# Performance work log

Measured on AMD Instinct MI355X. Metric: run time of the kernel, lower is better.

## Reference

```python
import jax, jax.numpy as jnp
import numpy as np

C = 66  # channels (joints)
NB_CLASSES = 14
T = 96


def conv1d(x, w, b, pad, groups=1):
    # x: (N, Cin, L), w: (Cout, Cin//groups, K)
    y = jax.lax.conv_general_dilated(
        x, w, window_strides=(1,), padding=[(pad, pad)],
        feature_group_count=groups, dimension_numbers=('NCH', 'OIH', 'NCH'))
    return y + b[None, :, None]


def pool2(x):
    # AvgPool1d(kernel_size=2) along last axis
    return x.reshape(*x.shape[:-1], x.shape[-1] // 2, 2).mean(-1)


def setup_inputs() -> dict:
    key = jax.random.key(0)
    ks = jax.random.split(key, 16)

    def xavier(k, shape, fan_in, fan_out, gain=jnp.sqrt(2.0)):
        bound = gain * jnp.sqrt(6.0 / (fan_in + fan_out))
        return jax.random.uniform(k, shape, jnp.float32, -bound, bound)

    B = 2048
    x = jax.random.normal(ks[0], (B, T, C), jnp.float32)
    # shared convs (same weights for every channel)
    w_hs = xavier(ks[1], (8, 1, 7), 1 * 7, 8 * 7)
    b_hs = jnp.full((8,), 0.1, jnp.float32)
    w_ls = xavier(ks[2], (8, 1, 3), 1 * 3, 8 * 3)
    b_ls = jnp.full((8,), 0.1, jnp.float32)
    # per-channel individual convs, packed for grouped conv (groups=C)
    w_hi1 = xavier(ks[3], (C * 4, 8, 7), 8 * 7, 4 * 7)
    b_hi1 = jnp.full((C * 4,), 0.1, jnp.float32)
    w_hi2 = xavier(ks[4], (C * 4, 4, 7), 4 * 7, 4 * 7)
    b_hi2 = jnp.full((C * 4,), 0.1, jnp.float32)
    w_li1 = xavier(ks[5], (C * 4, 8, 3), 8 * 3, 4 * 3)
    b_li1 = jnp.full((C * 4,), 0.1, jnp.float32)
    w_li2 = xavier(ks[6], (C * 4, 4, 3), 4 * 3, 4 * 3)
    b_li2 = jnp.full((C * 4,), 0.1, jnp.float32)
    # MLP
    F_IN = 9 * C * 12
    w_fc1 = xavier(ks[7], (1936, F_IN), F_IN, 1936)
    b_fc1 = jnp.full((1936,), 0.1, jnp.float32)
    w_fc2 = xavier(ks[8], (NB_CLASSES, 1936), 1936, NB_CLASSES)
    b_fc2 = jnp.full((NB_CLASSES,), 0.1, jnp.float32)
    return dict(x=x, w_hs=w_hs, b_hs=b_hs, w_ls=w_ls, b_ls=b_ls,
                w_hi1=w_hi1, b_hi1=b_hi1, w_hi2=w_hi2, b_hi2=b_hi2,
                w_li1=w_li1, b_li1=b_li1, w_li2=w_li2, b_li2=b_li2,
                w_fc1=w_fc1, b_fc1=b_fc1, w_fc2=w_fc2, b_fc2=b_fc2)


def _branch(xc_flat, B, w_s, b_s, w_i1, b_i1, w_i2, b_i2, pad):
    # xc_flat: (B*C, 1, T). Shared conv applied per channel, then grouped
    # (per-channel) convs with groups=C.
    h = pool2(jax.nn.relu(conv1d(xc_flat, w_s, b_s, pad)))       # (B*C, 8, 48)
    h = h.reshape(B, C * 8, T // 2)
    h = pool2(jax.nn.relu(conv1d(h, w_i1, b_i1, pad, groups=C)))  # (B, C*4, 24)
    h = pool2(jax.nn.relu(conv1d(h, w_i2, b_i2, pad, groups=C)))  # (B, C*4, 12)
    return h.reshape(B, C, 4, T // 8)


def reference(x, w_hs, b_hs, w_ls, b_ls, w_hi1, b_hi1, w_hi2, b_hi2,
              w_li1, b_li1, w_li2, b_li2, w_fc1, b_fc1, w_fc2, b_fc2):
    B = x.shape[0]
    xc = jnp.transpose(x, (0, 2, 1))            # (B, C, T)
    xc_flat = xc.reshape(B * C, 1, T)
    high = _branch(xc_flat, B, w_hs, b_hs, w_hi1, b_hi1, w_hi2, b_hi2, pad=3)
    low = _branch(xc_flat, B, w_ls, b_ls, w_li1, b_li1, w_li2, b_li2, pad=1)
    orig = pool2(pool2(pool2(xc)))[:, :, None, :]  # (B, C, 1, 12)
    # per-channel concat order: [original, low, high] -> (B, C, 9, 12)
    feat = jnp.concatenate([orig, low, high], axis=2).reshape(B, 9 * C * 12)
    h = jax.nn.relu(feat @ w_fc1.T + b_fc1)
    return h @ w_fc2.T + b_fc2
```

## Files before the change

kernel.cpp:

```cpp
#include <hip/hip_runtime.h>
#include <hip/hip_bf16.h>

#define T_LEN 96
#define C_CH  66
#define FIN   7128
#define KPAD  7168
#define NFC1  1936
#define NPAD  2048
#define NCLS  14

typedef __bf16 bf16x8 __attribute__((ext_vector_type(8)));
typedef float  f32x4  __attribute__((ext_vector_type(4)));

#define GLD_LDS(gp, lp) __builtin_amdgcn_global_load_lds(                     \
    (__attribute__((address_space(1))) void*)(gp),                            \
    (__attribute__((address_space(3))) void*)(lp), 16, 0, 0)

__global__ __launch_bounds__(256) void transpose_kernel(
    const float* __restrict__ x, float* __restrict__ xT, int B)
{
    __shared__ float tile[64][65];
    const int t = threadIdx.x & 63;
    const int w = threadIdx.x >> 6;
    const int tc0 = blockIdx.x * 64;
    const int b0  = blockIdx.y * 64;
    #pragma unroll
    for (int j = 0; j < 16; j++) {
        const int r = w * 16 + j;
        tile[r][t] = x[(size_t)(b0 + r) * (T_LEN * C_CH) + tc0 + t];
    }
    __syncthreads();
    #pragma unroll
    for (int j = 0; j < 16; j++) {
        const int r = w * 16 + j;
        xT[(size_t)(tc0 + r) * B + b0 + t] = tile[t][r];
    }
}

__global__ __launch_bounds__(256) void pad_w_kernel(
    const float* __restrict__ w, __hip_bfloat16* __restrict__ wb)
{
    int idx = blockIdx.x * 256 + threadIdx.x;
    int row = idx / 896;
    int cc  = idx - row * 896;
    float4 a = {0.f, 0.f, 0.f, 0.f}, b = {0.f, 0.f, 0.f, 0.f};
    if (row < NFC1 && cc < 891) {
        const float4* src = (const float4*)(w + (size_t)row * FIN + cc * 8);
        a = src[0];
        b = src[1];
    }
    __align__(16) __hip_bfloat16 v[8];
    v[0] = __float2bfloat16(a.x); v[1] = __float2bfloat16(a.y);
    v[2] = __float2bfloat16(a.z); v[3] = __float2bfloat16(a.w);
    v[4] = __float2bfloat16(b.x); v[5] = __float2bfloat16(b.y);
    v[6] = __float2bfloat16(b.z); v[7] = __float2bfloat16(b.w);
    *(int4*)(wb + (size_t)row * KPAD + cc * 8) = *(const int4*)v;
}

template <int K, bool DO_EXTRA>
__device__ __forceinline__ void conv_branch(
    const float* __restrict__ xb, int ts,
    const float* __restrict__ wS, const float* __restrict__ bS,
    const float* __restrict__ wi1, const float* __restrict__ bi1,
    const float* __restrict__ wi2, const float* __restrict__ bi2,
    __hip_bfloat16* __restrict__ frow, int out_off)
{
    constexpr int PAD = K / 2;
    constexpr int XW  = 24 + 6 * PAD;
    constexpr int THW = 12 + 2 * PAD;

    float s2phR[4][24];

    #pragma unroll
    for (int tt = 0; tt < 4; tt++) {
        float xw[XW];
        #pragma unroll
        for (int i = 0; i < XW; i++) {
            const int t = 24 * tt - 3 * PAD + i;
            xw[i] = (t >= 0 && t < T_LEN) ? xb[(size_t)t * ts] : 0.f;
        }

        if (DO_EXTRA) {
            #pragma unroll
            for (int r = 0; r < 3; r++) {
                float s = 0.f;
                #pragma unroll
                for (int k = 0; k < 8; k++) s += xw[3 * PAD + 8 * r + k];
                frow[3 * tt + r] = __float2bfloat16(s * 0.125f);
            }
        }

        float s2a[4][12];
        #pragma unroll
        for (int oc = 0; oc < 4; oc++) {
            const float bv = bi1[oc];
            #pragma unroll
            for (int q = 0; q < 12; q++) s2a[oc][q] = bv;
        }

        #pragma unroll 1
        for (int ic = 0; ic < 8; ic++) {
            const float bs1 = bS[ic];
            float thw[THW];
            #pragma unroll
            for (int j = 0; j < THW; j++) {
                const int jg = 12 * tt - PAD + j;
                if (jg < 0 || jg >= 48) { thw[j] = 0.f; continue; }
                float y0 = bs1, y1 = bs1;
                #pragma unroll
                for (int k = 0; k < K; k++) {
                    const float w = wS[ic * K + k];
                    y0 = fmaf(w, xw[2 * j + k], y0);
                    y1 = fmaf(w, xw[2 * j + 1 + k], y1);
                }
                thw[j] = 0.5f * (fmaxf(y0, 0.f) + fmaxf(y1, 0.f));
            }
            #pragma unroll
            for (int q = 0; q < 12; q++) {
                #pragma unroll
                for (int oc = 0; oc < 4; oc++) {
                    float a = s2a[oc][q];
                    #pragma unroll
                    for (int k = 0; k < K; k++)
                        a = fmaf(wi1[(oc * 8 + ic) * K + k], thw[q + k], a);
                    s2a[oc][q] = a;
                }
            }
        }

        #pragma unroll
        for (int oc = 0; oc < 4; oc++)
            #pragma unroll
            for (int r = 0; r < 6; r++)
                s2phR[oc][6 * tt + r] =
                    0.5f * (fmaxf(s2a[oc][2 * r], 0.f) +
                            fmaxf(s2a[oc][2 * r + 1], 0.f));
    }

    #pragma unroll 1
    for (int oc = 0; oc < 4; oc++) {
        const float bv = bi2[oc];
        #pragma unroll
        for (int q = 0; q < 12; q++) {
            float y0 = bv, y1 = bv;
            #pragma unroll
            for (int ic = 0; ic < 4; ic++) {
                #pragma unroll
                for (int k = 0; k < K; k++) {
                    const float w = wi2[(oc * 4 + ic) * K + k];
                    const int i0 = 2 * q + k - PAD;
                    const int i1 = 2 * q + 1 + k - PAD;
                    if (i0 >= 0 && i0 < 24) y0 = fmaf(w, s2phR[ic][i0], y0);
                    if (i1 >= 0 && i1 < 24) y1 = fmaf(w, s2phR[ic][i1], y1);
                }
            }
            frow[out_off + oc * 12 + q] =
                __float2bfloat16(0.5f * (fmaxf(y0, 0.f) + fmaxf(y1, 0.f)));
        }
    }
}

__global__ __launch_bounds__(64, 2) void conv_fused_kernel(
    const float* __restrict__ x, int ts, int bs, int cs,
    const float* __restrict__ w_hs, const float* __restrict__ b_hs,
    const float* __restrict__ w_ls, const float* __restrict__ b_ls,
    const float* __restrict__ w_hi1, const float* __restrict__ b_hi1,
    const float* __restrict__ w_hi2, const float* __restrict__ b_hi2,
    const float* __restrict__ w_li1, const float* __restrict__ b_li1,
    const float* __restrict__ w_li2, const float* __restrict__ b_li2,
    __hip_bfloat16* __restrict__ feat)
{
    const int lane = threadIdx.x;
    const int b = blockIdx.x * 64 + lane;
    const int c = blockIdx.y;
    const float* xb = x + (size_t)b * bs + (size_t)c * cs;
    __hip_bfloat16* frow = feat + (size_t)b * KPAD + c * 108;

    if (blockIdx.z == 0) {
        conv_branch<7, false>(xb, ts, w_hs, b_hs,
                              w_hi1 + c * 224, b_hi1 + c * 4,
                              w_hi2 + c * 112, b_hi2 + c * 4, frow, 60);
    } else {
        if (c == 0) {
            int4* tail = (int4*)(feat + (size_t)b * KPAD + FIN);
            const int4 z = {0, 0, 0, 0};
            #pragma unroll
            for (int i = 0; i < 5; i++) tail[i] = z;
        }
        conv_branch<3, true>(xb, ts, w_ls, b_ls,
                             w_li1 + c * 96, b_li1 + c * 4,
                             w_li2 + c * 48, b_li2 + c * 4, frow, 12);
    }
}

__global__ __launch_bounds__(512, 2) void gemm_kernel(
    const __hip_bfloat16* __restrict__ A,
    const __hip_bfloat16* __restrict__ Bw,
    float* __restrict__ Cm, int kchunk)
{
    __shared__ __align__(16) __hip_bfloat16 lds[2][2][256 * 64];

    const int tid  = threadIdx.x;
    const int lane = tid & 63;
    const int wid  = tid >> 6;
    const int m0 = blockIdx.y * 256;
    const int n0 = blockIdx.x * 256;
    const int wm = (wid >> 2) * 128;
    const int wn = (wid & 3) * 64;
    const int lr = lane & 15;
    const int quad = lane >> 4;

    const int srow = tid >> 3, scol = (tid & 7) * 8;
    const __hip_bfloat16* gA = A  + (size_t)(m0 + srow) * KPAD + scol;
    const __hip_bfloat16* gB = Bw + (size_t)(n0 + srow) * KPAD + scol;

    f32x4 acc[8][4] = {};

    const int kBeg = blockIdx.z * kchunk;
    const int numt = kchunk >> 6;

    #pragma unroll
    for (int r = 0; r < 4; r++) {
        GLD_LDS(gA + (size_t)r * 64 * KPAD + kBeg,
                &lds[0][0][r * 4096 + wid * 512]);
        GLD_LDS(gB + (size_t)r * 64 * KPAD + kBeg,
                &lds[0][1][r * 4096 + wid * 512]);
    }
    __syncthreads();

    for (int t = 0; t < numt; ++t) {
        const int cb = t & 1;
        if (t + 1 < numt) {
            const int k1 = kBeg + (t + 1) * 64;
            #pragma unroll
            for (int r = 0; r < 4; r++) {
                GLD_LDS(gA + (size_t)r * 64 * KPAD + k1,
                        &lds[cb ^ 1][0][r * 4096 + wid * 512]);
                GLD_LDS(gB + (size_t)r * 64 * KPAD + k1,
                        &lds[cb ^ 1][1][r * 4096 + wid * 512]);
            }
            asm volatile("s_waitcnt vmcnt(8)" ::: "memory");
        } else {
            asm volatile("s_waitcnt vmcnt(0)" ::: "memory");
        }
        __builtin_amdgcn_sched_barrier(0);
        __builtin_amdgcn_s_barrier();

        const __hip_bfloat16* As_ = &lds[cb][0][0];
        const __hip_bfloat16* Bs_ = &lds[cb][1][0];
        #pragma unroll
        for (int ks = 0; ks < 2; ks++) {
            bf16x8 bfr[4];
            #pragma unroll
            for (int nn = 0; nn < 4; nn++)
                bfr[nn] = *(const bf16x8*)(Bs_ + ((wn + nn * 16 + lr) << 6) +
                                           ks * 32 + quad * 8);
            #pragma unroll
            for (int mt = 0; mt < 8; mt++) {
                const bf16x8 af = *(const bf16x8*)(As_ +
                        ((wm + mt * 16 + lr) << 6) + ks * 32 + quad * 8);
                #pragma unroll
                for (int nn = 0; nn < 4; nn++)
                    acc[mt][nn] = __builtin_amdgcn_mfma_f32_16x16x32_bf16(
                        af, bfr[nn], acc[mt][nn], 0, 0, 0);
            }
        }
        __builtin_amdgcn_s_barrier();
    }

    float* Cs = Cm + (size_t)blockIdx.z * NPAD * NPAD;
    #pragma unroll
    for (int mt = 0; mt < 8; mt++) {
        #pragma unroll
        for (int nn = 0; nn < 4; nn++) {
            const int col = n0 + wn + nn * 16 + lr;
            const int rb  = m0 + wm + mt * 16 + quad * 4;
            #pragma unroll
            for (int r = 0; r < 4; r++)
                Cs[(size_t)(rb + r) * NPAD + col] = acc[mt][nn][r];
        }
    }
}

__global__ __launch_bounds__(256) void fc2_kernel(
    const float* __restrict__ h1, const float* __restrict__ b1,
    const float* __restrict__ w2, const float* __restrict__ b2,
    float* __restrict__ out, int nslab)
{
    const int b = blockIdx.x;
    const int tid = threadIdx.x;
    float acc[NCLS];
    #pragma unroll
    for (int o = 0; o < NCLS; o++) acc[o] = 0.f;
    for (int n = tid; n < NFC1; n += 256) {
        float hv = b1[n];
        for (int s = 0; s < nslab; s++)
            hv += h1[(size_t)s * NPAD * NPAD + (size_t)b * NPAD + n];
        float h = fmaxf(hv, 0.f);
        #pragma unroll
        for (int o = 0; o < NCLS; o++)
            acc[o] = fmaf(h, w2[o * NFC1 + n], acc[o]);
    }
    __shared__ float red[4][NCLS];
    #pragma unroll
    for (int o = 0; o < NCLS; o++) {
        float v = acc[o];
        #pragma unroll
        for (int s = 32; s > 0; s >>= 1) v += __shfl_down(v, s);
        if ((tid & 63) == 0) red[tid >> 6][o] = v;
    }
    __syncthreads();
    if (tid < NCLS)
        out[b * NCLS + tid] = red[0][tid] + red[1][tid] + red[2][tid] +
                              red[3][tid] + b2[tid];
}

extern "C" void kernel_launch(void* const* d_in, const int* in_sizes, int n_in,
                              void* d_out, int out_size, void* d_ws, size_t ws_size,
                              hipStream_t stream)
{
    (void)n_in; (void)out_size;
    const float* x     = (const float*)d_in[0];
    const float* w_hs  = (const float*)d_in[1];
    const float* b_hs  = (const float*)d_in[2];
    const float* w_ls  = (const float*)d_in[3];
    const float* b_ls  = (const float*)d_in[4];
    const float* w_hi1 = (const float*)d_in[5];
    const float* b_hi1 = (const float*)d_in[6];
    const float* w_hi2 = (const float*)d_in[7];
    const float* b_hi2 = (const float*)d_in[8];
    const float* w_li1 = (const float*)d_in[9];
    const float* b_li1 = (const float*)d_in[10];
    const float* w_li2 = (const float*)d_in[11];
    const float* b_li2 = (const float*)d_in[12];
    const float* w_fc1 = (const float*)d_in[13];
    const float* b_fc1 = (const float*)d_in[14];
    const float* w_fc2 = (const float*)d_in[15];
    const float* b_fc2 = (const float*)d_in[16];
    float* out = (float*)d_out;

    const int B = in_sizes[0] / (T_LEN * C_CH);

    char* ws = (char*)d_ws;
    const size_t featB = (size_t)B * KPAD * 2;
    const size_t wbB   = (size_t)NPAD * KPAD * 2;
    const size_t slabB = (size_t)NPAD * NPAD * 4;
    const size_t xtB   = (size_t)T_LEN * C_CH * B * 4;
    const size_t base2 = featB + wbB;

    __hip_bfloat16* feat = (__hip_bfloat16*)ws;
    __hip_bfloat16* wb   = (__hip_bfloat16*)(ws + featB);
    float* h1            = (float*)(ws + base2);

    const int sk = (ws_size >= base2 + 4 * slabB) ? 4 : 2;
    const bool use_xt = (ws_size >= base2 + sk * slabB + xtB);
    float* xT = (float*)(ws + base2 + sk * slabB);

    pad_w_kernel<<<dim3((NPAD * 896) / 256), 256, 0, stream>>>(w_fc1, wb);

    const float* cx = x;
    int ts = C_CH, bsi = T_LEN * C_CH, cs = 1;
    if (use_xt) {
        transpose_kernel<<<dim3(99, B / 64), 256, 0, stream>>>(x, xT, B);
        cx = xT; ts = C_CH * B; bsi = 1; cs = B;
    }
    conv_fused_kernel<<<dim3(B / 64, C_CH, 2), 64, 0, stream>>>(
        cx, ts, bsi, cs, w_hs, b_hs, w_ls, b_ls,
        w_hi1, b_hi1, w_hi2, b_hi2, w_li1, b_li1, w_li2, b_li2, feat);
    gemm_kernel<<<dim3(NPAD / 256, B / 256, sk), 512, 0, stream>>>(
        feat, wb, h1, KPAD / sk);
    fc2_kernel<<<dim3(B), 256, 0, stream>>>(h1, b_fc1, w_fc2, b_fc2, out, sk);
}
```

Baseline: 419.9 us.

## Split GEMM k-tile into half stages and interleave prefetch with MFMA

Restructures the GEMM LDS layout into per-k-half buffers of 32 columns and issues the next tile's global-to-LDS loads in quarter pieces between MFMA groups instead of all at once. Each k-half gets its own wait and barrier, and setprio raises priority around the MFMA bursts. The aim is finer-grained overlap of memory traffic with compute and less stall at the barrier. In exchange there are more barriers per tile and tighter waitcnt bookkeeping, which could be fragile if the vmcnt counts are wrong.

```diff
diff --git a/kernel.cpp b/kernel.cpp
--- a/kernel.cpp
+++ b/kernel.cpp
@@ -198,7 +198,7 @@
     const __hip_bfloat16* __restrict__ Bw,
     float* __restrict__ Cm, int kchunk)
 {
-    __shared__ __align__(16) __hip_bfloat16 lds[2][2][256 * 64];
+    __shared__ __align__(16) __hip_bfloat16 lds[2][2][2][8192];
 
     const int tid  = threadIdx.x;
     const int lane = tid & 63;
@@ -210,7 +210,7 @@
     const int lr = lane & 15;
     const int quad = lane >> 4;
 
-    const int srow = tid >> 3, scol = (tid & 7) * 8;
+    const int srow = tid >> 2, scol = (tid & 3) * 8;
     const __hip_bfloat16* gA = A  + (size_t)(m0 + srow) * KPAD + scol;
     const __hip_bfloat16* gB = Bw + (size_t)(n0 + srow) * KPAD + scol;
 
@@ -219,54 +219,104 @@
     const int kBeg = blockIdx.z * kchunk;
     const int numt = kchunk >> 6;
 
-    #pragma unroll
-    for (int r = 0; r < 4; r++) {
-        GLD_LDS(gA + (size_t)r * 64 * KPAD + kBeg,
-                &lds[0][0][r * 4096 + wid * 512]);
-        GLD_LDS(gB + (size_t)r * 64 * KPAD + kBeg,
-                &lds[0][1][r * 4096 + wid * 512]);
-    }
-    __syncthreads();
+#define STAGE_H(opidx, gptr, kh, kt)                                          \
+    do {                                                                      \
+        const size_t co = (size_t)(kBeg + (kt) * 64 + (kh) * 32);             \
+        GLD_LDS((gptr) + co, &lds[(kt) & 1][opidx][kh][wid * 512]);           \
+        GLD_LDS((gptr) + co + (size_t)128 * KPAD,                             \
+                &lds[(kt) & 1][opidx][kh][4096 + wid * 512]);                 \
+    } while (0)
+
+    STAGE_H(0, gA, 0, 0);
+    STAGE_H(1, gB, 0, 0);
+    STAGE_H(0, gA, 1, 0);
+    STAGE_H(1, gB, 1, 0);
 
     for (int t = 0; t < numt; ++t) {
-        const int cb = t & 1;
-        if (t + 1 < numt) {
-            const int k1 = kBeg + (t + 1) * 64;
-            #pragma unroll
-            for (int r = 0; r < 4; r++) {
-                GLD_LDS(gA + (size_t)r * 64 * KPAD + k1,
-                        &lds[cb ^ 1][0][r * 4096 + wid * 512]);
-                GLD_LDS(gB + (size_t)r * 64 * KPAD + k1,
-                        &lds[cb ^ 1][1][r * 4096 + wid * 512]);
-            }
-            asm volatile("s_waitcnt vmcnt(8)" ::: "memory");
-        } else {
-            asm volatile("s_waitcnt vmcnt(0)" ::: "memory");
-        }
+        const int p = t & 1;
+        const bool pf = (t + 1 < numt);
+
+        if (pf) asm volatile("s_waitcnt vmcnt(4)" ::: "memory");
+        else    asm volatile("s_waitcnt vmcnt(0)" ::: "memory");
         __builtin_amdgcn_sched_barrier(0);
         __builtin_amdgcn_s_barrier();
-
-        const __hip_bfloat16* As_ = &lds[cb][0][0];
-        const __hip_bfloat16* Bs_ = &lds[cb][1][0];
-        #pragma unroll
-        for (int ks = 0; ks < 2; ks++) {
-            bf16x8 bfr[4];
+        __builtin_amdgcn_sched_barrier(0);
+        {
+            bf16x8 bfr[4], af[4];
             #pragma unroll
             for (int nn = 0; nn < 4; nn++)
-                bfr[nn] = *(const bf16x8*)(Bs_ + ((wn + nn * 16 + lr) << 6) +
-                                           ks * 32 + quad * 8);
-            #pragma unroll
-            for (int mt = 0; mt < 8; mt++) {
-                const bf16x8 af = *(const bf16x8*)(As_ +
-                        ((wm + mt * 16 + lr) << 6) + ks * 32 + quad * 8);
+                bfr[nn] = *(const bf16x8*)&lds[p][1][0][
+                    (wn + nn * 16 + lr) * 32 + quad * 8];
+            #pragma unroll
+            for (int i = 0; i < 4; i++)
+                af[i] = *(const bf16x8*)&lds[p][0][0][
+                    (wm + i * 16 + lr) * 32 + quad * 8];
+            if (pf) STAGE_H(0, gA, 0, t + 1);
+            __builtin_amdgcn_s_setprio(1);
+            #pragma unroll
+            for (int i = 0; i < 4; i++)
                 #pragma unroll
                 for (int nn = 0; nn < 4; nn++)
-                    acc[mt][nn] = __builtin_amdgcn_mfma_f32_16x16x32_bf16(
-                        af, bfr[nn], acc[mt][nn], 0, 0, 0);
-            }
-        }
+                    acc[i][nn] = __builtin_amdgcn_mfma_f32_16x16x32_bf16(
+                        af[i], bfr[nn], acc[i][nn], 0, 0, 0);
+            __builtin_amdgcn_s_setprio(0);
+
+            #pragma unroll
+            for (int i = 0; i < 4; i++)
+                af[i] = *(const bf16x8*)&lds[p][0][0][
+                    (wm + 64 + i * 16 + lr) * 32 + quad * 8];
+            if (pf) STAGE_H(1, gB, 0, t + 1);
+            __builtin_amdgcn_s_setprio(1);
+            #pragma unroll
+            for (int i = 0; i < 4; i++)
+                #pragma unroll
+                for (int nn = 0; nn < 4; nn++)
+                    acc[4 + i][nn] = __builtin_amdgcn_mfma_f32_16x16x32_bf16(
+                        af[i], bfr[nn], acc[4 + i][nn], 0, 0, 0);
+            __builtin_amdgcn_s_setprio(0);
+        }
+
+        if (pf) asm volatile("s_waitcnt vmcnt(4)" ::: "memory");
+        else    asm volatile("s_waitcnt vmcnt(0)" ::: "memory");
+        __builtin_amdgcn_sched_barrier(0);
         __builtin_amdgcn_s_barrier();
-    }
+        __builtin_amdgcn_sched_barrier(0);
+        {
+            bf16x8 bfr[4], af[4];
+            #pragma unroll
+            for (int nn = 0; nn < 4; nn++)
+                bfr[nn] = *(const bf16x8*)&lds[p][1][1][
+                    (wn + nn * 16 + lr) * 32 + quad * 8];
+            #pragma unroll
+            for (int i = 0; i < 4; i++)
+                af[i] = *(const bf16x8*)&lds[p][0][1][
+                    (wm + i * 16 + lr) * 32 + quad * 8];
+            if (pf) STAGE_H(0, gA, 1, t + 1);
+            __builtin_amdgcn_s_setprio(1);
+            #pragma unroll
+            for (int i = 0; i < 4; i++)
+                #pragma unroll
+                for (int nn = 0; nn < 4; nn++)
+                    acc[i][nn] = __builtin_amdgcn_mfma_f32_16x16x32_bf16(
+                        af[i], bfr[nn], acc[i][nn], 0, 0, 0);
+            __builtin_amdgcn_s_setprio(0);
+
+            #pragma unroll
+            for (int i = 0; i < 4; i++)
+                af[i] = *(const bf16x8*)&lds[p][0][1][
+                    (wm + 64 + i * 16 + lr) * 32 + quad * 8];
+            if (pf) STAGE_H(1, gB, 1, t + 1);
+            __builtin_amdgcn_s_setprio(1);
+            #pragma unroll
+            for (int i = 0; i < 4; i++)
+                #pragma unroll
+                for (int nn = 0; nn < 4; nn++)
+                    acc[4 + i][nn] = __builtin_amdgcn_mfma_f32_16x16x32_bf16(
+                        af[i], bfr[nn], acc[4 + i][nn], 0, 0, 0);
+            __builtin_amdgcn_s_setprio(0);
+        }
+    }
+#undef STAGE_H
 
     float* Cs = Cm + (size_t)blockIdx.z * NPAD * NPAD;
     #pragma unroll
```

Result: faster. 402.6 us (-4.1%).
